# Kernel tuning notes

Measured on AMD Instinct MI355X. Metric: run time of the kernel, lower is better.

The kernel has to match this reference:

```python
import jax, jax.numpy as jnp
import numpy as np

N = 100000      # nodes
E = 1600000     # directed edges (avg degree 16)
D_IN, D_H, D_OUT = 128, 128, 1


def gcn_conv(x, src, dst, W, b, n):
    """PyG GCNConv: out = D^{-1/2} (A+I) D^{-1/2} X W + b.
    src/dst already include self-loops. deg counted on dst (in-degree)."""
    h = x @ W                                            # [n, d_out]
    deg = jax.ops.segment_sum(jnp.ones(src.shape[0], h.dtype), dst, num_segments=n)
    dinv = jax.lax.rsqrt(jnp.maximum(deg, 1.0))          # deg >= 1 (self loops)
    norm = dinv[src] * dinv[dst]                         # [e]
    msg = h[src] * norm[:, None]                         # gather + scale, [e, d_out]
    out = jax.ops.segment_sum(msg, dst, num_segments=n)  # scatter-add, [n, d_out]
    return out + b


def setup_inputs() -> dict:
    key = jax.random.key(0)
    ks = jax.random.split(key, 8)
    x = jax.random.normal(ks[0], (N, D_IN), dtype=jnp.float32)
    edge_index = jax.random.randint(ks[1], (2, E), 0, N, dtype=jnp.int64)

    def glorot(k, fan_in, fan_out):
        s = jnp.sqrt(6.0 / (fan_in + fan_out)).astype(jnp.float32)
        return jax.random.uniform(k, (fan_in, fan_out), jnp.float32, -s, s)

    W0 = glorot(ks[2], D_IN, D_H)
    b0 = jnp.zeros((D_H,), jnp.float32)
    W1 = glorot(ks[3], D_H, D_H)
    b1 = jnp.zeros((D_H,), jnp.float32)
    W2 = glorot(ks[4], D_H, D_OUT)
    b2 = jnp.zeros((D_OUT,), jnp.float32)
    return {"x": x, "edge_index": edge_index,
            "W0": W0, "b0": b0, "W1": W1, "b1": b1, "W2": W2, "b2": b2}


def reference(x, edge_index, W0, b0, W1, b1, W2, b2):
    n = x.shape[0]
    loops = jnp.arange(n, dtype=edge_index.dtype)
    src = jnp.concatenate([edge_index[0], loops])
    dst = jnp.concatenate([edge_index[1], loops])
    # dropout is identity in eval mode
    h = jax.nn.relu(gcn_conv(x, src, dst, W0, b0, n))
    h = jax.nn.relu(gcn_conv(h, src, dst, W1, b1, n))
    out = gcn_conv(h, src, dst, W2, b2, n)
    return jax.nn.sigmoid(out)
```

## Files before the change

kernel.cpp:

```cpp
#include <hip/hip_runtime.h>
#include <cstddef>

#define D 128
#define BW_LOG 11
#define BW 2048
#define CHUNK 8192
#define GP 136
typedef unsigned int uint;
typedef unsigned short ushort;

typedef __attribute__((ext_vector_type(8))) short bf16x8;
typedef __attribute__((ext_vector_type(4))) float f32x4;

static __device__ __forceinline__ uint bf16r(float x) {
  uint u = __float_as_uint(x);
  return (u + 0x7fffu + ((u >> 16) & 1u)) >> 16;
}
static __device__ __forceinline__ uint pack2(float a, float b) {
  return bf16r(a) | (bf16r(b) << 16);
}
static __device__ __forceinline__ void acc_bf16x8(const uint4 v, float* a) {
  a[0] += __uint_as_float(v.x << 16);
  a[1] += __uint_as_float(v.x & 0xffff0000u);
  a[2] += __uint_as_float(v.y << 16);
  a[3] += __uint_as_float(v.y & 0xffff0000u);
  a[4] += __uint_as_float(v.z << 16);
  a[5] += __uint_as_float(v.z & 0xffff0000u);
  a[6] += __uint_as_float(v.w << 16);
  a[7] += __uint_as_float(v.w & 0xffff0000u);
}

__global__ void k_bzero(int* __restrict__ bcnt, int nb) {
  int t = threadIdx.x;
  if (t < nb) bcnt[t] = 0;
}

__global__ __launch_bounds__(512)
void k_bhist(const int* __restrict__ dstA, int* __restrict__ bcnt, int e, int nb) {
  __shared__ int h[256];
  int t = threadIdx.x;
  if (t < nb) h[t] = 0;
  __syncthreads();
  int base = blockIdx.x * CHUNK;
  int m = min(CHUNK, e - base);
  for (int i = t; i < m; i += 512) atomicAdd(&h[dstA[base + i] >> BW_LOG], 1);
  __syncthreads();
  if (t < nb && h[t]) atomicAdd(&bcnt[t], h[t]);
}

__global__ void k_bscan(const int* __restrict__ bcnt, int* __restrict__ bbase,
                        int* __restrict__ cursor, int* __restrict__ off,
                        int nb, int n, int e) {
  __shared__ int s[256];
  int t = threadIdx.x;
  int v = (t < nb) ? bcnt[t] : 0;
  s[t] = v;
  __syncthreads();
  for (int d = 1; d < 256; d <<= 1) {
    int x = (t >= d) ? s[t - d] : 0;
    __syncthreads();
    s[t] += x;
    __syncthreads();
  }
  if (t < nb) {
    int b = s[t] - v;
    bbase[t] = b;
    cursor[t] = b;
  }
  if (t == 0) {
    bbase[nb] = e;
    off[n] = e;
  }
}

__global__ __launch_bounds__(512)
void k_bscatter(const int* __restrict__ ei, int* __restrict__ cursor,
                int* __restrict__ pk, int e, int nb) {
  __shared__ int h[256], lbase[256], gpos[256], lcur[256], s2[256];
  __shared__ int staged[CHUNK];
  int t = threadIdx.x;
  if (t < nb) h[t] = 0;
  __syncthreads();
  int base = blockIdx.x * CHUNK;
  int m = min(CHUNK, e - base);
  int sv[16], dv[16];
#pragma unroll
  for (int k = 0; k < 16; ++k) {
    int i = t + k * 512;
    sv[k] = 0; dv[k] = 0;
    if (i < m) {
      sv[k] = ei[base + i];
      dv[k] = ei[e + base + i];
      atomicAdd(&h[dv[k] >> BW_LOG], 1);
    }
  }
  __syncthreads();
  if (t < 256) s2[t] = (t < nb) ? h[t] : 0;
  __syncthreads();
  for (int d = 1; d < 256; d <<= 1) {
    int x = 0;
    if (t < 256 && t >= d) x = s2[t - d];
    __syncthreads();
    if (t < 256) s2[t] += x;
    __syncthreads();
  }
  if (t < nb) {
    lbase[t] = s2[t] - h[t];
    lcur[t] = s2[t] - h[t];
    gpos[t] = h[t] ? atomicAdd(&cursor[t], h[t]) : 0;
  }
  __syncthreads();
#pragma unroll
  for (int k = 0; k < 16; ++k) {
    int i = t + k * 512;
    if (i < m) {
      int b = dv[k] >> BW_LOG;
      int p = atomicAdd(&lcur[b], 1);
      staged[p] = sv[k] | ((dv[k] & (BW - 1)) << 17);
    }
  }
  __syncthreads();
  for (int b = 0; b < nb; ++b) {
    int cnt = h[b], lb = lbase[b], gp = gpos[b];
    for (int i = t; i < cnt; i += 512) pk[gp + i] = staged[lb + i];
  }
}

__global__ __launch_bounds__(1024)
void k_bfinal(const int* __restrict__ bbase, const int* __restrict__ pk,
              int* __restrict__ off, float* __restrict__ dinv,
              int* __restrict__ csr, int n, int nb) {
  __shared__ int sc[BW];
  __shared__ int lcur[BW];
  const int b = blockIdx.x;
  const int t = threadIdx.x;
  const int e0 = bbase[b], e1 = bbase[b + 1];
  const int node0 = b << BW_LOG;
  sc[t] = 0; sc[t + 1024] = 0;
  lcur[t] = 0; lcur[t + 1024] = 0;
  __syncthreads();
  for (int i = e0 + t; i < e1; i += 1024) atomicAdd(&sc[(pk[i] >> 17) & (BW - 1)], 1);
  __syncthreads();
  int c0 = sc[t], c1 = sc[t + 1024];
  for (int d = 1; d < BW; d <<= 1) {
    int v0 = (t >= d) ? sc[t - d] : 0;
    int v1 = (t + 1024 >= d) ? sc[t + 1024 - d] : 0;
    __syncthreads();
    sc[t] += v0; sc[t + 1024] += v1;
    __syncthreads();
  }
  int ex0 = sc[t] - c0, ex1 = sc[t + 1024] - c1;
  int na = node0 + t, nbn = node0 + t + 1024;
  if (na < n)  { off[na]  = e0 + ex0; dinv[na]  = rsqrtf((float)c0 + 1.0f); }
  if (nbn < n) { off[nbn] = e0 + ex1; dinv[nbn] = rsqrtf((float)c1 + 1.0f); }
  __syncthreads();
  sc[t] = ex0; sc[t + 1024] = ex1;
  __syncthreads();
  for (int i = e0 + t; i < e1; i += 1024) {
    int v = pk[i];
    int dl = (v >> 17) & (BW - 1);
    int p = atomicAdd(&lcur[dl], 1);
    csr[e0 + sc[dl] + p] = v & 0x1FFFF;
  }
}

template <bool RELU_BIAS>
__global__ __launch_bounds__(256)
void k_mgemm(const float* __restrict__ X, const float* __restrict__ W,
             const float* __restrict__ bias, const float* __restrict__ dinv,
             ushort* __restrict__ Asb, int n, int nstrips) {
  __shared__ __align__(16) ushort Wh[128 * GP];
  __shared__ __align__(16) ushort Wl[128 * GP];
  const int tid = threadIdx.x;

  for (int i = tid; i < 4096; i += 256) {
    int nn = i & 127;
    int k0 = (i >> 7) * 4;
    union { ushort4 v; ushort a[4]; } h, l;
#pragma unroll
    for (int r = 0; r < 4; ++r) {
      float w = W[(size_t)(k0 + r) * D + nn];
      uint hb = bf16r(w);
      float hf = __uint_as_float(hb << 16);
      h.a[r] = (ushort)hb;
      l.a[r] = (ushort)bf16r(w - hf);
    }
    *(ushort4*)(&Wh[nn * GP + k0]) = h.v;
    *(ushort4*)(&Wl[nn * GP + k0]) = l.v;
  }
  __syncthreads();

  const int wv = tid >> 6;
  const int l = tid & 63;
  const int lr = l & 15;
  const int lk = (l >> 4) * 8;

  for (int strip = blockIdx.x * 4 + wv; strip < nstrips; strip += gridDim.x * 4) {
    const int row0 = strip * 16;
    f32x4 acc[8];
#pragma unroll
    for (int t = 0; t < 8; ++t) acc[t] = (f32x4){0.f, 0.f, 0.f, 0.f};

    const int arow = row0 + lr;
    const bool av = (arow < n);
    const float* ap = X + (size_t)arow * D;

#pragma unroll
    for (int ks = 0; ks < 4; ++ks) {
      const int k0 = ks * 32 + lk;
      float a8[8];
      if (av) {
        float4 u0 = *(const float4*)(ap + k0);
        float4 u1 = *(const float4*)(ap + k0 + 4);
        a8[0] = u0.x; a8[1] = u0.y; a8[2] = u0.z; a8[3] = u0.w;
        a8[4] = u1.x; a8[5] = u1.y; a8[6] = u1.z; a8[7] = u1.w;
        if (RELU_BIAS) {
          float4 b0v = *(const float4*)(bias + k0);
          float4 b1v = *(const float4*)(bias + k0 + 4);
          a8[0] = fmaxf(a8[0] + b0v.x, 0.f);
          a8[1] = fmaxf(a8[1] + b0v.y, 0.f);
          a8[2] = fmaxf(a8[2] + b0v.z, 0.f);
          a8[3] = fmaxf(a8[3] + b0v.w, 0.f);
          a8[4] = fmaxf(a8[4] + b1v.x, 0.f);
          a8[5] = fmaxf(a8[5] + b1v.y, 0.f);
          a8[6] = fmaxf(a8[6] + b1v.z, 0.f);
          a8[7] = fmaxf(a8[7] + b1v.w, 0.f);
        }
      } else {
#pragma unroll
        for (int j = 0; j < 8; ++j) a8[j] = 0.f;
      }
      union { bf16x8 v; ushort a[8]; } ah, al;
#pragma unroll
      for (int j = 0; j < 8; ++j) {
        uint hb = bf16r(a8[j]);
        float hf = __uint_as_float(hb << 16);
        ah.a[j] = (ushort)hb;
        al.a[j] = (ushort)bf16r(a8[j] - hf);
      }
#pragma unroll
      for (int nt = 0; nt < 8; ++nt) {
        bf16x8 bh = *(const bf16x8*)(&Wh[(nt * 16 + lr) * GP + k0]);
        bf16x8 bl = *(const bf16x8*)(&Wl[(nt * 16 + lr) * GP + k0]);
        acc[nt] = __builtin_amdgcn_mfma_f32_16x16x32_bf16(ah.v, bh, acc[nt], 0, 0, 0);
        acc[nt] = __builtin_amdgcn_mfma_f32_16x16x32_bf16(al.v, bh, acc[nt], 0, 0, 0);
        acc[nt] = __builtin_amdgcn_mfma_f32_16x16x32_bf16(ah.v, bl, acc[nt], 0, 0, 0);
      }
    }

#pragma unroll
    for (int r = 0; r < 4; ++r) {
      int row = row0 + (l >> 4) * 4 + r;
      if (row < n) {
        float di = dinv[row];
#pragma unroll
        for (int nt = 0; nt < 8; ++nt) {
          Asb[(size_t)row * D + nt * 16 + lr] = (ushort)bf16r(acc[nt][r] * di);
        }
      }
    }
  }
}

template <bool FUSE_DOT>
__global__ __launch_bounds__(256)
void k_gather(const int* __restrict__ off, const int* __restrict__ csr,
              const float* __restrict__ dinv, const ushort* __restrict__ Asb,
              float* __restrict__ B, const float* __restrict__ b1,
              const float* __restrict__ W2, float* __restrict__ ss, int n) {
  const int wid = blockIdx.x * 4 + (threadIdx.x >> 6);
  if (wid >= n) return;
  const int lane = threadIdx.x & 63;
  const int q = lane >> 4;
  const int li = lane & 15;
  const int c = li << 3;

  float a[8];
#pragma unroll
  for (int k = 0; k < 8; ++k) a[k] = 0.f;
  if (q == 0) {
    uint4 sv = *(const uint4*)(Asb + (size_t)wid * D + c);
    acc_bf16x8(sv, a);
  }

  const int o0 = off[wid], o1 = off[wid + 1];
  for (int j0 = o0; j0 < o1; j0 += 64) {
    int sj = 0;
    if (j0 + lane < o1) sj = csr[j0 + lane];
    const int m = min(64, o1 - j0);
    const int nst = (m + 3) >> 2;
#pragma unroll 4
    for (int t = 0; t < nst; ++t) {
      int idx = (t << 2) + q;
      int s = __shfl(sj, idx);
      if (idx < m) {
        uint4 v = *(const uint4*)(Asb + (size_t)s * D + c);
        acc_bf16x8(v, a);
      }
    }
  }

#pragma unroll
  for (int k = 0; k < 8; ++k) {
    a[k] += __shfl_xor(a[k], 16);
    a[k] += __shfl_xor(a[k], 32);
  }

  const float di = dinv[wid];
  if (FUSE_DOT) {
    float4 bb0 = *(const float4*)(b1 + c);
    float4 bb1 = *(const float4*)(b1 + c + 4);
    float4 w0 = *(const float4*)(W2 + c);
    float4 w1 = *(const float4*)(W2 + c + 4);
    float p = 0.f;
    p += fmaxf(a[0] * di + bb0.x, 0.f) * w0.x;
    p += fmaxf(a[1] * di + bb0.y, 0.f) * w0.y;
    p += fmaxf(a[2] * di + bb0.z, 0.f) * w0.z;
    p += fmaxf(a[3] * di + bb0.w, 0.f) * w0.w;
    p += fmaxf(a[4] * di + bb1.x, 0.f) * w1.x;
    p += fmaxf(a[5] * di + bb1.y, 0.f) * w1.y;
    p += fmaxf(a[6] * di + bb1.z, 0.f) * w1.z;
    p += fmaxf(a[7] * di + bb1.w, 0.f) * w1.w;
    p += __shfl_xor(p, 1);
    p += __shfl_xor(p, 2);
    p += __shfl_xor(p, 4);
    p += __shfl_xor(p, 8);
    if (lane == 0) ss[wid] = p * di;
  } else {
    if (lane < 16) {
      float4 o0v = make_float4(a[0] * di, a[1] * di, a[2] * di, a[3] * di);
      float4 o1v = make_float4(a[4] * di, a[5] * di, a[6] * di, a[7] * di);
      *(float4*)(B + (size_t)wid * D + c)     = o0v;
      *(float4*)(B + (size_t)wid * D + c + 4) = o1v;
    }
  }
}

__global__ void k_gather_scalar(const int* __restrict__ off, const int* __restrict__ csr,
                                const float* __restrict__ dinv, const float* __restrict__ ss,
                                const float* __restrict__ b2, float* __restrict__ out, int n) {
  int i = blockIdx.x * 256 + threadIdx.x;
  if (i >= n) return;
  float acc = ss[i];
  int j = off[i], o1 = off[i + 1];
  float a0 = 0.f, a1 = 0.f, a2 = 0.f, a3 = 0.f;
  for (; j + 4 <= o1; j += 4) {
    int s0 = csr[j], s1 = csr[j + 1], s2 = csr[j + 2], s3 = csr[j + 3];
    a0 += ss[s0];
    a1 += ss[s1];
    a2 += ss[s2];
    a3 += ss[s3];
  }
  for (; j < o1; ++j) a0 += ss[csr[j]];
  acc += (a0 + a1) + (a2 + a3);
  float v = acc * dinv[i] + b2[0];
  out[i] = 1.f / (1.f + expf(-v));
}

extern "C" void kernel_launch(void* const* d_in, const int* in_sizes, int n_in,
                              void* d_out, int out_size, void* d_ws, size_t ws_size,
                              hipStream_t stream) {
  const float* x  = (const float*)d_in[0];
  const int*   ei = (const int*)d_in[1];
  const float* W0 = (const float*)d_in[2];
  const float* b0 = (const float*)d_in[3];
  const float* W1 = (const float*)d_in[4];
  const float* b1 = (const float*)d_in[5];
  const float* W2 = (const float*)d_in[6];
  const float* b2 = (const float*)d_in[7];
  float* out = (float*)d_out;

  const int n = in_sizes[0] / D;
  const int e = in_sizes[1] / 2;
  const int nb = (n + BW - 1) / BW;
  const int nstrips = (n + 15) / 16;
  const size_t np = ((size_t)n + 256) / 256 * 256;

  float* ws = (float*)d_ws;
  int*    off    = (int*)ws;
  float*  dinv   = ws + np;
  float*  ss     = ws + 2 * np;
  int*    bmeta  = (int*)(ws + 3 * np);
  int*    bcnt   = bmeta;
  int*    bbase  = bmeta + 260;
  int*    cursor = bmeta + 600;
  int*    csr    = (int*)(ws + 3 * np + 1024);
  int*    pk     = csr + e;
  ushort* Asb    = (ushort*)(pk + e);
  float*  B      = (float*)(Asb + (size_t)n * D);

  const int g256n = (n + 255) / 256;
  const int ggath = (n + 3) / 4;
  const int gchnk = (e + CHUNK - 1) / CHUNK;

  k_bzero<<<1, 256, 0, stream>>>(bcnt, nb);
  k_bhist<<<gchnk, 512, 0, stream>>>(ei + e, bcnt, e, nb);
  k_bscan<<<1, 256, 0, stream>>>(bcnt, bbase, cursor, off, nb, n, e);
  k_bscatter<<<gchnk, 512, 0, stream>>>(ei, cursor, pk, e, nb);
  k_bfinal<<<nb, 1024, 0, stream>>>(bbase, pk, off, dinv, csr, n, nb);

  k_mgemm<false><<<512, 256, 0, stream>>>(x, W0, nullptr, dinv, Asb, n, nstrips);
  k_gather<false><<<ggath, 256, 0, stream>>>(off, csr, dinv, Asb, B, nullptr, nullptr, nullptr, n);

  k_mgemm<true><<<512, 256, 0, stream>>>(B, W1, b0, dinv, Asb, n, nstrips);
  k_gather<true><<<ggath, 256, 0, stream>>>(off, csr, dinv, Asb, nullptr, b1, W2, ss, n);

  k_gather_scalar<<<g256n, 256, 0, stream>>>(off, csr, dinv, ss, b2, out, n);
}
```

Before: 294.8 us.

## Store layer-1 activations as bf16 with fused bias/ReLU, enlarge GEMM blocks

The first aggregation kernel now applies bias and ReLU itself and writes the hidden activations as bf16 instead of fp32. The second GEMM reads these bf16 rows directly, so it needs only two split-bf16 MFMAs per tile instead of three. The intent is to halve the activation write/read traffic and cut MFMA work in the second layer. GEMM blocks also grow to 512 threads, with one strip per wave and a grid sized to cover all strips. The cost is extra rounding error, since the hidden layer is no longer held in fp32 precision.

```diff
diff --git a/kernel.cpp b/kernel.cpp
--- a/kernel.cpp
+++ b/kernel.cpp
@@ -164,16 +164,15 @@
   }
 }
 
-template <bool RELU_BIAS>
-__global__ __launch_bounds__(256)
-void k_mgemm(const float* __restrict__ X, const float* __restrict__ W,
-             const float* __restrict__ bias, const float* __restrict__ dinv,
-             ushort* __restrict__ Asb, int n, int nstrips) {
+__global__ __launch_bounds__(512)
+void k_mgemm_f32(const float* __restrict__ X, const float* __restrict__ W,
+                 const float* __restrict__ dinv, ushort* __restrict__ Asb,
+                 int n, int nstrips) {
   __shared__ __align__(16) ushort Wh[128 * GP];
   __shared__ __align__(16) ushort Wl[128 * GP];
   const int tid = threadIdx.x;
 
-  for (int i = tid; i < 4096; i += 256) {
+  for (int i = tid; i < 4096; i += 512) {
     int nn = i & 127;
     int k0 = (i >> 7) * 4;
     union { ushort4 v; ushort a[4]; } h, l;
@@ -195,7 +194,7 @@
   const int lr = l & 15;
   const int lk = (l >> 4) * 8;
 
-  for (int strip = blockIdx.x * 4 + wv; strip < nstrips; strip += gridDim.x * 4) {
+  for (int strip = blockIdx.x * 8 + wv; strip < nstrips; strip += gridDim.x * 8) {
     const int row0 = strip * 16;
     f32x4 acc[8];
 #pragma unroll
@@ -214,18 +213,6 @@
         float4 u1 = *(const float4*)(ap + k0 + 4);
         a8[0] = u0.x; a8[1] = u0.y; a8[2] = u0.z; a8[3] = u0.w;
         a8[4] = u1.x; a8[5] = u1.y; a8[6] = u1.z; a8[7] = u1.w;
-        if (RELU_BIAS) {
-          float4 b0v = *(const float4*)(bias + k0);
-          float4 b1v = *(const float4*)(bias + k0 + 4);
-          a8[0] = fmaxf(a8[0] + b0v.x, 0.f);
-          a8[1] = fmaxf(a8[1] + b0v.y, 0.f);
-          a8[2] = fmaxf(a8[2] + b0v.z, 0.f);
-          a8[3] = fmaxf(a8[3] + b0v.w, 0.f);
-          a8[4] = fmaxf(a8[4] + b1v.x, 0.f);
-          a8[5] = fmaxf(a8[5] + b1v.y, 0.f);
-          a8[6] = fmaxf(a8[6] + b1v.z, 0.f);
-          a8[7] = fmaxf(a8[7] + b1v.w, 0.f);
-        }
       } else {
 #pragma unroll
         for (int j = 0; j < 8; ++j) a8[j] = 0.f;
@@ -262,11 +249,86 @@
   }
 }
 
+__global__ __launch_bounds__(512)
+void k_mgemm_bf(const ushort* __restrict__ Xb, const float* __restrict__ W,
+                const float* __restrict__ dinv, ushort* __restrict__ Asb,
+                int n, int nstrips) {
+  __shared__ __align__(16) ushort Wh[128 * GP];
+  __shared__ __align__(16) ushort Wl[128 * GP];
+  const int tid = threadIdx.x;
+
+  for (int i = tid; i < 4096; i += 512) {
+    int nn = i & 127;
+    int k0 = (i >> 7) * 4;
+    union { ushort4 v; ushort a[4]; } h, l;
+#pragma unroll
+    for (int r = 0; r < 4; ++r) {
+      float w = W[(size_t)(k0 + r) * D + nn];
+      uint hb = bf16r(w);
+      float hf = __uint_as_float(hb << 16);
+      h.a[r] = (ushort)hb;
+      l.a[r] = (ushort)bf16r(w - hf);
+    }
+    *(ushort4*)(&Wh[nn * GP + k0]) = h.v;
+    *(ushort4*)(&Wl[nn * GP + k0]) = l.v;
+  }
+  __syncthreads();
+
+  const int wv = tid >> 6;
+  const int l = tid & 63;
+  const int lr = l & 15;
+  const int lk = (l >> 4) * 8;
+
+  for (int strip = blockIdx.x * 8 + wv; strip < nstrips; strip += gridDim.x * 8) {
+    const int row0 = strip * 16;
+    f32x4 acc[8];
+#pragma unroll
+    for (int t = 0; t < 8; ++t) acc[t] = (f32x4){0.f, 0.f, 0.f, 0.f};
+
+    const int arow = row0 + lr;
+    const bool av = (arow < n);
+    const ushort* ap = Xb + (size_t)arow * D;
+
+#pragma unroll
+    for (int ks = 0; ks < 4; ++ks) {
+      const int k0 = ks * 32 + lk;
+      bf16x8 ah;
+      if (av) {
+        ah = *(const bf16x8*)(ap + k0);
+      } else {
+        union { bf16x8 v; ushort a[8]; } z;
+#pragma unroll
+        for (int j = 0; j < 8; ++j) z.a[j] = 0;
+        ah = z.v;
+      }
+#pragma unroll
+      for (int nt = 0; nt < 8; ++nt) {
+        bf16x8 bh = *(const bf16x8*)(&Wh[(nt * 16 + lr) * GP + k0]);
+        bf16x8 bl = *(const bf16x8*)(&Wl[(nt * 16 + lr) * GP + k0]);
+        acc[nt] = __builtin_amdgcn_mfma_f32_16x16x32_bf16(ah, bh, acc[nt], 0, 0, 0);
+        acc[nt] = __builtin_amdgcn_mfma_f32_16x16x32_bf16(ah, bl, acc[nt], 0, 0, 0);
+      }
+    }
+
+#pragma unroll
+    for (int r = 0; r < 4; ++r) {
+      int row = row0 + (l >> 4) * 4 + r;
+      if (row < n) {
+        float di = dinv[row];
+#pragma unroll
+        for (int nt = 0; nt < 8; ++nt) {
+          Asb[(size_t)row * D + nt * 16 + lr] = (ushort)bf16r(acc[nt][r] * di);
+        }
+      }
+    }
+  }
+}
+
 template <bool FUSE_DOT>
 __global__ __launch_bounds__(256)
 void k_gather(const int* __restrict__ off, const int* __restrict__ csr,
               const float* __restrict__ dinv, const ushort* __restrict__ Asb,
-              float* __restrict__ B, const float* __restrict__ b1,
+              ushort* __restrict__ Bb, const float* __restrict__ bias,
               const float* __restrict__ W2, float* __restrict__ ss, int n) {
   const int wid = blockIdx.x * 4 + (threadIdx.x >> 6);
   if (wid >= n) return;
@@ -307,20 +369,22 @@
   }
 
   const float di = dinv[wid];
+  float4 bb0 = *(const float4*)(bias + c);
+  float4 bb1 = *(const float4*)(bias + c + 4);
+  float v0 = fmaxf(a[0] * di + bb0.x, 0.f);
+  float v1 = fmaxf(a[1] * di + bb0.y, 0.f);
+  float v2 = fmaxf(a[2] * di + bb0.z, 0.f);
+  float v3 = fmaxf(a[3] * di + bb0.w, 0.f);
+  float v4 = fmaxf(a[4] * di + bb1.x, 0.f);
+  float v5 = fmaxf(a[5] * di + bb1.y, 0.f);
+  float v6 = fmaxf(a[6] * di + bb1.z, 0.f);
+  float v7 = fmaxf(a[7] * di + bb1.w, 0.f);
+
   if (FUSE_DOT) {
-    float4 bb0 = *(const float4*)(b1 + c);
-    float4 bb1 = *(const float4*)(b1 + c + 4);
     float4 w0 = *(const float4*)(W2 + c);
     float4 w1 = *(const float4*)(W2 + c + 4);
-    float p = 0.f;
-    p += fmaxf(a[0] * di + bb0.x, 0.f) * w0.x;
-    p += fmaxf(a[1] * di + bb0.y, 0.f) * w0.y;
-    p += fmaxf(a[2] * di + bb0.z, 0.f) * w0.z;
-    p += fmaxf(a[3] * di + bb0.w, 0.f) * w0.w;
-    p += fmaxf(a[4] * di + bb1.x, 0.f) * w1.x;
-    p += fmaxf(a[5] * di + bb1.y, 0.f) * w1.y;
-    p += fmaxf(a[6] * di + bb1.z, 0.f) * w1.z;
-    p += fmaxf(a[7] * di + bb1.w, 0.f) * w1.w;
+    float p = v0 * w0.x + v1 * w0.y + v2 * w0.z + v3 * w0.w +
+              v4 * w1.x + v5 * w1.y + v6 * w1.z + v7 * w1.w;
     p += __shfl_xor(p, 1);
     p += __shfl_xor(p, 2);
     p += __shfl_xor(p, 4);
@@ -328,10 +392,12 @@
     if (lane == 0) ss[wid] = p * di;
   } else {
     if (lane < 16) {
-      float4 o0v = make_float4(a[0] * di, a[1] * di, a[2] * di, a[3] * di);
-      float4 o1v = make_float4(a[4] * di, a[5] * di, a[6] * di, a[7] * di);
-      *(float4*)(B + (size_t)wid * D + c)     = o0v;
-      *(float4*)(B + (size_t)wid * D + c + 4) = o1v;
+      uint4 w;
+      w.x = pack2(v0, v1);
+      w.y = pack2(v2, v3);
+      w.z = pack2(v4, v5);
+      w.w = pack2(v6, v7);
+      *(uint4*)(Bb + (size_t)wid * D + c) = w;
     }
   }
 }
@@ -387,11 +453,12 @@
   int*    csr    = (int*)(ws + 3 * np + 1024);
   int*    pk     = csr + e;
   ushort* Asb    = (ushort*)(pk + e);
-  float*  B      = (float*)(Asb + (size_t)n * D);
+  ushort* Bb     = Asb + (size_t)n * D;
 
   const int g256n = (n + 255) / 256;
   const int ggath = (n + 3) / 4;
   const int gchnk = (e + CHUNK - 1) / CHUNK;
+  const int ggemm = (nstrips + 7) / 8;
 
   k_bzero<<<1, 256, 0, stream>>>(bcnt, nb);
   k_bhist<<<gchnk, 512, 0, stream>>>(ei + e, bcnt, e, nb);
@@ -399,10 +466,10 @@
   k_bscatter<<<gchnk, 512, 0, stream>>>(ei, cursor, pk, e, nb);
   k_bfinal<<<nb, 1024, 0, stream>>>(bbase, pk, off, dinv, csr, n, nb);
 
-  k_mgemm<false><<<512, 256, 0, stream>>>(x, W0, nullptr, dinv, Asb, n, nstrips);
-  k_gather<false><<<ggath, 256, 0, stream>>>(off, csr, dinv, Asb, B, nullptr, nullptr, nullptr, n);
-
-  k_mgemm<true><<<512, 256, 0, stream>>>(B, W1, b0, dinv, Asb, n, nstrips);
+  k_mgemm_f32<<<ggemm, 512, 0, stream>>>(x, W0, dinv, Asb, n, nstrips);
+  k_gather<false><<<ggath, 256, 0, stream>>>(off, csr, dinv, Asb, Bb, b0, nullptr, nullptr, n);
+
+  k_mgemm_bf<<<ggemm, 512, 0, stream>>>(Bb, W1, dinv, Asb, n, nstrips);
   k_gather<true><<<ggath, 256, 0, stream>>>(off, csr, dinv, Asb, nullptr, b1, W2, ss, n);
 
   k_gather_scalar<<<g256n, 256, 0, stream>>>(off, csr, dinv, ss, b2, out, n);
```

Measured after the change: 361.4 us. 22.6% more time.

## Store layer-1 activations as bf16, fuse bias/relu into gather, presplit weights

Applied to the files above, without the earlier changes.

The first gather now applies bias and ReLU itself and writes the hidden activations as bf16 instead of fp32, so the second GEMM reads half the bytes and drops the low-part A MFMA. The weight hi/lo bf16 split moves into a separate one-time kernel. The GEMM keeps only the hi part in LDS and reads the lo part from global memory. The GEMM grid is also resized to match the strip count. The cost is lower precision for the layer-2 input, which is now bf16 rounded instead of a split fp32, plus an extra small kernel launch.

```diff
diff --git a/kernel.cpp b/kernel.cpp
--- a/kernel.cpp
+++ b/kernel.cpp
@@ -164,29 +164,31 @@
   }
 }
 
-template <bool RELU_BIAS>
+__global__ void k_wsplit(const float* __restrict__ W0, const float* __restrict__ W1,
+                         ushort* __restrict__ out) {
+  int idx = blockIdx.x * 256 + threadIdx.x;
+  if (idx >= 32768) return;
+  int lay = idx >> 14;
+  int rem = idx & 16383;
+  int col = rem >> 7, k = rem & 127;
+  const float* W = lay ? W1 : W0;
+  float w = W[k * D + col];
+  uint hb = bf16r(w);
+  float hf = __uint_as_float(hb << 16);
+  out[lay * 32768 + rem] = (ushort)hb;
+  out[lay * 32768 + 16384 + rem] = (ushort)bf16r(w - hf);
+}
+
+template <bool BF16A>
 __global__ __launch_bounds__(256)
-void k_mgemm(const float* __restrict__ X, const float* __restrict__ W,
-             const float* __restrict__ bias, const float* __restrict__ dinv,
+void k_mgemm(const void* __restrict__ Xv, const ushort* __restrict__ Wht,
+             const ushort* __restrict__ Wlt, const float* __restrict__ dinv,
              ushort* __restrict__ Asb, int n, int nstrips) {
   __shared__ __align__(16) ushort Wh[128 * GP];
-  __shared__ __align__(16) ushort Wl[128 * GP];
   const int tid = threadIdx.x;
 
-  for (int i = tid; i < 4096; i += 256) {
-    int nn = i & 127;
-    int k0 = (i >> 7) * 4;
-    union { ushort4 v; ushort a[4]; } h, l;
-#pragma unroll
-    for (int r = 0; r < 4; ++r) {
-      float w = W[(size_t)(k0 + r) * D + nn];
-      uint hb = bf16r(w);
-      float hf = __uint_as_float(hb << 16);
-      h.a[r] = (ushort)hb;
-      l.a[r] = (ushort)bf16r(w - hf);
-    }
-    *(ushort4*)(&Wh[nn * GP + k0]) = h.v;
-    *(ushort4*)(&Wl[nn * GP + k0]) = l.v;
+  for (int c = tid; c < 2048; c += 256) {
+    *(uint4*)(&Wh[(c >> 4) * GP + (c & 15) * 8]) = *(const uint4*)(Wht + c * 8);
   }
   __syncthreads();
 
@@ -195,6 +197,9 @@
   const int lr = l & 15;
   const int lk = (l >> 4) * 8;
 
+  const float* Xf = (const float*)Xv;
+  const ushort* Xb = (const ushort*)Xv;
+
   for (int strip = blockIdx.x * 4 + wv; strip < nstrips; strip += gridDim.x * 4) {
     const int row0 = strip * 16;
     f32x4 acc[8];
@@ -203,48 +208,51 @@
 
     const int arow = row0 + lr;
     const bool av = (arow < n);
-    const float* ap = X + (size_t)arow * D;
 
 #pragma unroll
     for (int ks = 0; ks < 4; ++ks) {
       const int k0 = ks * 32 + lk;
-      float a8[8];
-      if (av) {
-        float4 u0 = *(const float4*)(ap + k0);
-        float4 u1 = *(const float4*)(ap + k0 + 4);
-        a8[0] = u0.x; a8[1] = u0.y; a8[2] = u0.z; a8[3] = u0.w;
-        a8[4] = u1.x; a8[5] = u1.y; a8[6] = u1.z; a8[7] = u1.w;
-        if (RELU_BIAS) {
-          float4 b0v = *(const float4*)(bias + k0);
-          float4 b1v = *(const float4*)(bias + k0 + 4);
-          a8[0] = fmaxf(a8[0] + b0v.x, 0.f);
-          a8[1] = fmaxf(a8[1] + b0v.y, 0.f);
-          a8[2] = fmaxf(a8[2] + b0v.z, 0.f);
-          a8[3] = fmaxf(a8[3] + b0v.w, 0.f);
-          a8[4] = fmaxf(a8[4] + b1v.x, 0.f);
-          a8[5] = fmaxf(a8[5] + b1v.y, 0.f);
-          a8[6] = fmaxf(a8[6] + b1v.z, 0.f);
-          a8[7] = fmaxf(a8[7] + b1v.w, 0.f);
+      bf16x8 ahv, alv;
+      if (BF16A) {
+        if (av) {
+          ahv = *(const bf16x8*)(Xb + (size_t)arow * D + k0);
+        } else {
+          union { bf16x8 v; ushort a[8]; } z;
+#pragma unroll
+          for (int j = 0; j < 8; ++j) z.a[j] = 0;
+          ahv = z.v;
         }
       } else {
-#pragma unroll
-        for (int j = 0; j < 8; ++j) a8[j] = 0.f;
-      }
-      union { bf16x8 v; ushort a[8]; } ah, al;
-#pragma unroll
-      for (int j = 0; j < 8; ++j) {
-        uint hb = bf16r(a8[j]);
-        float hf = __uint_as_float(hb << 16);
-        ah.a[j] = (ushort)hb;
-        al.a[j] = (ushort)bf16r(a8[j] - hf);
+        float a8[8];
+        if (av) {
+          const float* ap = Xf + (size_t)arow * D + k0;
+          float4 u0 = *(const float4*)(ap);
+          float4 u1 = *(const float4*)(ap + 4);
+          a8[0] = u0.x; a8[1] = u0.y; a8[2] = u0.z; a8[3] = u0.w;
+          a8[4] = u1.x; a8[5] = u1.y; a8[6] = u1.z; a8[7] = u1.w;
+        } else {
+#pragma unroll
+          for (int j = 0; j < 8; ++j) a8[j] = 0.f;
+        }
+        union { bf16x8 v; ushort a[8]; } ah, al;
+#pragma unroll
+        for (int j = 0; j < 8; ++j) {
+          uint hb = bf16r(a8[j]);
+          float hf = __uint_as_float(hb << 16);
+          ah.a[j] = (ushort)hb;
+          al.a[j] = (ushort)bf16r(a8[j] - hf);
+        }
+        ahv = ah.v;
+        alv = al.v;
       }
 #pragma unroll
       for (int nt = 0; nt < 8; ++nt) {
         bf16x8 bh = *(const bf16x8*)(&Wh[(nt * 16 + lr) * GP + k0]);
-        bf16x8 bl = *(const bf16x8*)(&Wl[(nt * 16 + lr) * GP + k0]);
-        acc[nt] = __builtin_amdgcn_mfma_f32_16x16x32_bf16(ah.v, bh, acc[nt], 0, 0, 0);
-        acc[nt] = __builtin_amdgcn_mfma_f32_16x16x32_bf16(al.v, bh, acc[nt], 0, 0, 0);
-        acc[nt] = __builtin_amdgcn_mfma_f32_16x16x32_bf16(ah.v, bl, acc[nt], 0, 0, 0);
+        bf16x8 bl = *(const bf16x8*)(Wlt + (size_t)(nt * 16 + lr) * D + k0);
+        acc[nt] = __builtin_amdgcn_mfma_f32_16x16x32_bf16(ahv, bh, acc[nt], 0, 0, 0);
+        if (!BF16A)
+          acc[nt] = __builtin_amdgcn_mfma_f32_16x16x32_bf16(alv, bh, acc[nt], 0, 0, 0);
+        acc[nt] = __builtin_amdgcn_mfma_f32_16x16x32_bf16(ahv, bl, acc[nt], 0, 0, 0);
       }
     }
 
@@ -266,7 +274,7 @@
 __global__ __launch_bounds__(256)
 void k_gather(const int* __restrict__ off, const int* __restrict__ csr,
               const float* __restrict__ dinv, const ushort* __restrict__ Asb,
-              float* __restrict__ B, const float* __restrict__ b1,
+              ushort* __restrict__ Bb, const float* __restrict__ bias,
               const float* __restrict__ W2, float* __restrict__ ss, int n) {
   const int wid = blockIdx.x * 4 + (threadIdx.x >> 6);
   if (wid >= n) return;
@@ -307,20 +315,22 @@
   }
 
   const float di = dinv[wid];
+  float4 bb0 = *(const float4*)(bias + c);
+  float4 bb1 = *(const float4*)(bias + c + 4);
+  float v0 = fmaxf(a[0] * di + bb0.x, 0.f);
+  float v1 = fmaxf(a[1] * di + bb0.y, 0.f);
+  float v2 = fmaxf(a[2] * di + bb0.z, 0.f);
+  float v3 = fmaxf(a[3] * di + bb0.w, 0.f);
+  float v4 = fmaxf(a[4] * di + bb1.x, 0.f);
+  float v5 = fmaxf(a[5] * di + bb1.y, 0.f);
+  float v6 = fmaxf(a[6] * di + bb1.z, 0.f);
+  float v7 = fmaxf(a[7] * di + bb1.w, 0.f);
+
   if (FUSE_DOT) {
-    float4 bb0 = *(const float4*)(b1 + c);
-    float4 bb1 = *(const float4*)(b1 + c + 4);
     float4 w0 = *(const float4*)(W2 + c);
     float4 w1 = *(const float4*)(W2 + c + 4);
-    float p = 0.f;
-    p += fmaxf(a[0] * di + bb0.x, 0.f) * w0.x;
-    p += fmaxf(a[1] * di + bb0.y, 0.f) * w0.y;
-    p += fmaxf(a[2] * di + bb0.z, 0.f) * w0.z;
-    p += fmaxf(a[3] * di + bb0.w, 0.f) * w0.w;
-    p += fmaxf(a[4] * di + bb1.x, 0.f) * w1.x;
-    p += fmaxf(a[5] * di + bb1.y, 0.f) * w1.y;
-    p += fmaxf(a[6] * di + bb1.z, 0.f) * w1.z;
-    p += fmaxf(a[7] * di + bb1.w, 0.f) * w1.w;
+    float p = v0 * w0.x + v1 * w0.y + v2 * w0.z + v3 * w0.w +
+              v4 * w1.x + v5 * w1.y + v6 * w1.z + v7 * w1.w;
     p += __shfl_xor(p, 1);
     p += __shfl_xor(p, 2);
     p += __shfl_xor(p, 4);
@@ -328,10 +338,12 @@
     if (lane == 0) ss[wid] = p * di;
   } else {
     if (lane < 16) {
-      float4 o0v = make_float4(a[0] * di, a[1] * di, a[2] * di, a[3] * di);
-      float4 o1v = make_float4(a[4] * di, a[5] * di, a[6] * di, a[7] * di);
-      *(float4*)(B + (size_t)wid * D + c)     = o0v;
-      *(float4*)(B + (size_t)wid * D + c + 4) = o1v;
+      uint4 w;
+      w.x = pack2(v0, v1);
+      w.y = pack2(v2, v3);
+      w.z = pack2(v4, v5);
+      w.w = pack2(v6, v7);
+      *(uint4*)(Bb + (size_t)wid * D + c) = w;
     }
   }
 }
@@ -384,25 +396,33 @@
   int*    bcnt   = bmeta;
   int*    bbase  = bmeta + 260;
   int*    cursor = bmeta + 600;
-  int*    csr    = (int*)(ws + 3 * np + 1024);
+  ushort* wsp    = (ushort*)(ws + 3 * np + 1024);
+  int*    csr    = (int*)(ws + 3 * np + 1024 + 32768);
   int*    pk     = csr + e;
   ushort* Asb    = (ushort*)(pk + e);
-  float*  B      = (float*)(Asb + (size_t)n * D);
+  ushort* Bb     = Asb + (size_t)n * D;
+
+  const ushort* W0h = wsp;
+  const ushort* W0l = wsp + 16384;
+  const ushort* W1h = wsp + 32768;
+  const ushort* W1l = wsp + 49152;
 
   const int g256n = (n + 255) / 256;
   const int ggath = (n + 3) / 4;
   const int gchnk = (e + CHUNK - 1) / CHUNK;
-
+  const int ggemm = (nstrips + 3) / 4 < 1024 ? (nstrips + 3) / 4 : 1024;
+
+  k_wsplit<<<128, 256, 0, stream>>>(W0, W1, (ushort*)wsp);
   k_bzero<<<1, 256, 0, stream>>>(bcnt, nb);
   k_bhist<<<gchnk, 512, 0, stream>>>(ei + e, bcnt, e, nb);
   k_bscan<<<1, 256, 0, stream>>>(bcnt, bbase, cursor, off, nb, n, e);
   k_bscatter<<<gchnk, 512, 0, stream>>>(ei, cursor, pk, e, nb);
   k_bfinal<<<nb, 1024, 0, stream>>>(bbase, pk, off, dinv, csr, n, nb);
 
-  k_mgemm<false><<<512, 256, 0, stream>>>(x, W0, nullptr, dinv, Asb, n, nstrips);
-  k_gather<false><<<ggath, 256, 0, stream>>>(off, csr, dinv, Asb, B, nullptr, nullptr, nullptr, n);
-
-  k_mgemm<true><<<512, 256, 0, stream>>>(B, W1, b0, dinv, Asb, n, nstrips);
+  k_mgemm<false><<<ggemm, 256, 0, stream>>>(x, W0h, W0l, dinv, Asb, n, nstrips);
+  k_gather<false><<<ggath, 256, 0, stream>>>(off, csr, dinv, Asb, Bb, b0, nullptr, nullptr, n);
+
+  k_mgemm<true><<<ggemm, 256, 0, stream>>>(Bb, W1h, W1l, dinv, Asb, n, nstrips);
   k_gather<true><<<ggath, 256, 0, stream>>>(off, csr, dinv, Asb, nullptr, b1, W2, ss, n);
 
   k_gather_scalar<<<g256n, 256, 0, stream>>>(off, csr, dinv, ss, b2, out, n);
```

Result: no change. 295.5 us (+0.3%).
